# Performance work log

Hardware: AMD Instinct MI355X
Metric: run time of the kernel (lower is better)

## Reference

```python
import jax, jax.numpy as jnp
import numpy as np

LN_EPS = 1e-5
ATTN_THRESH = 0.0005


def _layernorm(x, g, b):
    mu = jnp.mean(x, axis=-1, keepdims=True)
    var = jnp.mean((x - mu) ** 2, axis=-1, keepdims=True)
    return (x - mu) / jnp.sqrt(var + LN_EPS) * g + b


def setup_inputs() -> dict:
    key = jax.random.key(0)
    ks = jax.random.split(key, 10)
    B, P, X, C = 4, 1024, 8192, 1024
    return {
        "feat": jax.random.normal(ks[0], (B, P, C), dtype=jnp.float32),
        "mem_k": jax.random.normal(ks[1], (B, X, C), dtype=jnp.float32),
        "mem_v": jax.random.normal(ks[2], (B, X, C), dtype=jnp.float32),
        "mem_c": jax.random.uniform(ks[3], (B, X, 1), dtype=jnp.float32),
        "mem_attn": jnp.zeros((B, X, 1), dtype=jnp.float32),
        "g_q": jax.random.uniform(ks[4], (C,), dtype=jnp.float32, minval=0.5, maxval=1.5),
        "b_q": jax.random.normal(ks[5], (C,), dtype=jnp.float32) * 0.02,
        "g_k": jax.random.uniform(ks[6], (C,), dtype=jnp.float32, minval=0.5, maxval=1.5),
        "b_k": jax.random.normal(ks[7], (C,), dtype=jnp.float32) * 0.02,
        "g_v": jax.random.uniform(ks[8], (C,), dtype=jnp.float32, minval=0.5, maxval=1.5),
        "b_v": jax.random.normal(ks[9], (C,), dtype=jnp.float32) * 0.02,
    }


def reference(feat, mem_k, mem_v, mem_c, mem_attn, g_q, b_q, g_k, b_k, g_v, b_v):
    # SpatialMemory.memory_read with res=True
    C = feat.shape[-1]
    q = _layernorm(feat, g_q, b_q)                      # [B,P,C]
    k = _layernorm(mem_k, g_k, b_k)                     # [B,X,C]
    affinity = jnp.einsum('bpc,bxc->bpx', q, k)
    affinity = affinity / jnp.sqrt(jnp.asarray(C, jnp.float32))
    # confidence scaling: mem_c viewed as [B,1,X]
    affinity = affinity * jnp.swapaxes(mem_c, 1, 2)
    attn = jax.nn.softmax(affinity, axis=-1)            # [B,P,X]
    # threshold sparsify + renormalize
    attn = jnp.where(attn < ATTN_THRESH, jnp.zeros((), attn.dtype), attn)
    attn = attn / jnp.sum(attn, axis=-1, keepdims=True)
    v = _layernorm(mem_v, g_v, b_v)                     # [B,X,C]
    out = jnp.einsum('bpx,bxc->bpc', attn, v) + feat    # residual
    return out
```

## Files before the change

### kernel.cpp

```cpp
#include <hip/hip_runtime.h>

typedef __attribute__((ext_vector_type(8))) _Float16 half8;
typedef __attribute__((ext_vector_type(4))) _Float16 half4v;
typedef __attribute__((ext_vector_type(4))) float f32x4;

__device__ __forceinline__ void gll16(const void* g, void* l) {
  __builtin_amdgcn_global_load_lds(
      (const __attribute__((address_space(1))) unsigned int*)g,
      (__attribute__((address_space(3))) unsigned int*)l, 16, 0, 0);
}

__global__ __launch_bounds__(256) void ln_cast_f16(
    const float* __restrict__ x, const float* __restrict__ g,
    const float* __restrict__ b, _Float16* __restrict__ y) {
  const int C = 1024;
  size_t row = blockIdx.x;
  int t = threadIdx.x;
  const float4* xr = (const float4*)(x + row * C);
  float4 v = xr[t];
  float s = v.x + v.y + v.z + v.w;
  float s2 = v.x * v.x + v.y * v.y + v.z * v.z + v.w * v.w;
#pragma unroll
  for (int off = 1; off < 64; off <<= 1) {
    s += __shfl_xor(s, off, 64);
    s2 += __shfl_xor(s2, off, 64);
  }
  __shared__ float ps[4], ps2[4];
  int wave = t >> 6, lane = t & 63;
  if (lane == 0) { ps[wave] = s; ps2[wave] = s2; }
  __syncthreads();
  s = ps[0] + ps[1] + ps[2] + ps[3];
  s2 = ps2[0] + ps2[1] + ps2[2] + ps2[3];
  float mu = s * (1.0f / C);
  float var = s2 * (1.0f / C) - mu * mu;
  float rstd = rsqrtf(var + 1e-5f);
  float4 gv = ((const float4*)g)[t];
  float4 bv = ((const float4*)b)[t];
  half4v o;
  o.x = (_Float16)((v.x - mu) * rstd * gv.x + bv.x);
  o.y = (_Float16)((v.y - mu) * rstd * gv.y + bv.y);
  o.z = (_Float16)((v.z - mu) * rstd * gv.z + bv.z);
  o.w = (_Float16)((v.w - mu) * rstd * gv.w + bv.w);
  ((half4v*)(y + row * C))[t] = o;
}

__global__ __launch_bounds__(256) void gemm_bt_f16(
    const _Float16* __restrict__ A,
    const _Float16* __restrict__ Bm,
    float* __restrict__ Cm,
    int M, int N, int K,
    const float* __restrict__ colscale,
    float scale)
{
  int bz = blockIdx.z;
  const _Float16* Ab = A + (size_t)bz * M * K;
  const _Float16* Bb = Bm + (size_t)bz * N * K;
  float* Cb = Cm + (size_t)bz * M * N;

  __shared__ _Float16 lA[128 * 32];
  __shared__ _Float16 lB[128 * 32];

  int tid = threadIdx.x;
  int wave = tid >> 6, lane = tid & 63;
  int wm = wave >> 1, wn = wave & 1;
  int m0 = blockIdx.y * 128, n0 = blockIdx.x * 128;

  f32x4 acc[4][4];
  f32x4 zero = {0.f, 0.f, 0.f, 0.f};
#pragma unroll
  for (int i = 0; i < 4; ++i)
#pragma unroll
    for (int j = 0; j < 4; ++j) acc[i][j] = zero;

  int seg0 = wave * 2, seg1 = wave * 2 + 1;
  int row0 = (seg0 & 1) * 64 + lane, kc0 = seg0 >> 1;
  int row1 = (seg1 & 1) * 64 + lane, kc1 = seg1 >> 1;

  const _Float16* gA0 = Ab + (size_t)(m0 + row0) * K + kc0 * 8;
  const _Float16* gA1 = Ab + (size_t)(m0 + row1) * K + kc1 * 8;
  const _Float16* gB0 = Bb + (size_t)(n0 + row0) * K + kc0 * 8;
  const _Float16* gB1 = Bb + (size_t)(n0 + row1) * K + kc1 * 8;
  _Float16* dA0 = &lA[seg0 * 512 + lane * 8];
  _Float16* dA1 = &lA[seg1 * 512 + lane * 8];
  _Float16* dB0 = &lB[seg0 * 512 + lane * 8];
  _Float16* dB1 = &lB[seg1 * 512 + lane * 8];

  int kg = lane >> 4, lr = lane & 15;

  for (int k0 = 0; k0 < K; k0 += 32) {
    __syncthreads();
    gll16(gA0 + k0, dA0);
    gll16(gA1 + k0, dA1);
    gll16(gB0 + k0, dB0);
    gll16(gB1 + k0, dB1);
    __syncthreads();
    half8 af[4], bfr[4];
#pragma unroll
    for (int t = 0; t < 4; ++t) {
      int m = wm * 64 + t * 16 + lr;
      af[t] = *(const half8*)&lA[kg * 1024 + m * 8];
      int n = wn * 64 + t * 16 + lr;
      bfr[t] = *(const half8*)&lB[kg * 1024 + n * 8];
    }
#pragma unroll
    for (int t = 0; t < 4; ++t)
#pragma unroll
      for (int u = 0; u < 4; ++u)
        acc[t][u] = __builtin_amdgcn_mfma_f32_16x16x32_f16(af[t], bfr[u], acc[t][u], 0, 0, 0);
  }

  int cq = lane >> 4, cn = lane & 15;
  const float* csb = colscale ? colscale + (size_t)bz * N : nullptr;
#pragma unroll
  for (int u = 0; u < 4; ++u) {
    int gn = n0 + wn * 64 + u * 16 + cn;
    float cs = scale * (csb ? csb[gn] : 1.0f);
#pragma unroll
    for (int t = 0; t < 4; ++t) {
      int gm = m0 + wm * 64 + t * 16 + cq * 4;
#pragma unroll
      for (int r = 0; r < 4; ++r) {
        size_t idx = (size_t)(gm + r) * N + gn;
        Cb[idx] = acc[t][u][r] * cs;
      }
    }
  }
}

__global__ __launch_bounds__(256) void softmax_compact(
    const float* __restrict__ S, unsigned* __restrict__ entries,
    int* __restrict__ counts) {
  const int X = 8192;
  size_t row = blockIdx.x;
  const float4* sr = (const float4*)(S + row * X);
  int t = threadIdx.x;
  int wave = t >> 6, lane = t & 63;
  __shared__ float sh[4];
  __shared__ int scnt;
  float4 v[8];
#pragma unroll
  for (int j = 0; j < 8; ++j) v[j] = sr[t + j * 256];

  float m = -1e30f;
#pragma unroll
  for (int j = 0; j < 8; ++j)
    m = fmaxf(m, fmaxf(fmaxf(v[j].x, v[j].y), fmaxf(v[j].z, v[j].w)));
#pragma unroll
  for (int off = 1; off < 64; off <<= 1) m = fmaxf(m, __shfl_xor(m, off, 64));
  if (lane == 0) sh[wave] = m;
  __syncthreads();
  m = fmaxf(fmaxf(sh[0], sh[1]), fmaxf(sh[2], sh[3]));
  __syncthreads();

  float l = 0.f;
#pragma unroll
  for (int j = 0; j < 8; ++j) {
    v[j].x = __expf(v[j].x - m);
    v[j].y = __expf(v[j].y - m);
    v[j].z = __expf(v[j].z - m);
    v[j].w = __expf(v[j].w - m);
    l += v[j].x + v[j].y + v[j].z + v[j].w;
  }
#pragma unroll
  for (int off = 1; off < 64; off <<= 1) l += __shfl_xor(l, off, 64);
  if (lane == 0) sh[wave] = l;
  __syncthreads();
  l = sh[0] + sh[1] + sh[2] + sh[3];
  __syncthreads();

  float thr = 0.0005f * l;
  float ks = 0.f;
#pragma unroll
  for (int j = 0; j < 8; ++j) {
    v[j].x = (v[j].x >= thr) ? v[j].x : 0.f;
    v[j].y = (v[j].y >= thr) ? v[j].y : 0.f;
    v[j].z = (v[j].z >= thr) ? v[j].z : 0.f;
    v[j].w = (v[j].w >= thr) ? v[j].w : 0.f;
    ks += v[j].x + v[j].y + v[j].z + v[j].w;
  }
#pragma unroll
  for (int off = 1; off < 64; off <<= 1) ks += __shfl_xor(ks, off, 64);
  if (lane == 0) sh[wave] = ks;
  __syncthreads();
  if (t == 0) scnt = 0;
  __syncthreads();
  ks = sh[0] + sh[1] + sh[2] + sh[3];

  float inv = 1.0f / ks;
  unsigned* er = entries + row * 2048;
#pragma unroll
  for (int j = 0; j < 8; ++j) {
    int cbase = (t + j * 256) * 4;
    float vals[4] = {v[j].x, v[j].y, v[j].z, v[j].w};
#pragma unroll
    for (int c = 0; c < 4; ++c) {
      if (vals[c] > 0.f) {
        int pos = atomicAdd(&scnt, 1);
        _Float16 h = (_Float16)(vals[c] * inv);
        unsigned short hb;
        __builtin_memcpy(&hb, &h, 2);
        er[pos] = ((unsigned)(cbase + c) << 16) | hb;
      }
    }
  }
  __syncthreads();
  if (t == 0) counts[row] = scnt;
}

__global__ __launch_bounds__(256) void gather_pv(
    const unsigned* __restrict__ entries, const int* __restrict__ counts,
    const _Float16* __restrict__ v16, const float* __restrict__ feat,
    float* __restrict__ out) {
  const int X = 8192, C = 1024;
  int row = blockIdx.x;
  int b = row >> 10;
  const unsigned* er = entries + (size_t)row * 2048;
  int cnt = counts[row];
  int t = threadIdx.x;
  const _Float16* vb = v16 + (size_t)b * X * C;

  float4 acc = {0.f, 0.f, 0.f, 0.f};
  __shared__ unsigned se[256];

  for (int base = 0; base < cnt; base += 256) {
    int n = min(256, cnt - base);
    __syncthreads();
    if (t < n) se[t] = er[base + t];
    __syncthreads();
#pragma unroll 8
    for (int j = 0; j < n; ++j) {
      unsigned e = se[j];
      int x = e >> 16;
      unsigned short hb = (unsigned short)(e & 0xffff);
      _Float16 h;
      __builtin_memcpy(&h, &hb, 2);
      float w = (float)h;
      half4v vv = *(const half4v*)(vb + (size_t)x * C + t * 4);
      acc.x += w * (float)vv.x;
      acc.y += w * (float)vv.y;
      acc.z += w * (float)vv.z;
      acc.w += w * (float)vv.w;
    }
  }
  size_t o = (size_t)row * C + t * 4;
  float4 f = *(const float4*)(feat + o);
  acc.x += f.x; acc.y += f.y; acc.z += f.z; acc.w += f.w;
  *(float4*)(out + o) = acc;
}

extern "C" void kernel_launch(void* const* d_in, const int* in_sizes, int n_in,
                              void* d_out, int out_size, void* d_ws, size_t ws_size,
                              hipStream_t stream) {
  const int B = 4, P = 1024, X = 8192, C = 1024;
  const float* feat  = (const float*)d_in[0];
  const float* mem_k = (const float*)d_in[1];
  const float* mem_v = (const float*)d_in[2];
  const float* mem_c = (const float*)d_in[3];
  const float* g_q = (const float*)d_in[5];
  const float* b_q = (const float*)d_in[6];
  const float* g_k = (const float*)d_in[7];
  const float* b_k = (const float*)d_in[8];
  const float* g_v = (const float*)d_in[9];
  const float* b_v = (const float*)d_in[10];

  char* ws = (char*)d_ws;
  const size_t MB = 1024 * 1024;
  _Float16* q16 = (_Float16*)(ws + 0);
  _Float16* k16 = (_Float16*)(ws + 8 * MB);
  _Float16* v16 = (_Float16*)(ws + 72 * MB);
  float*    S   = (float*)(ws + 136 * MB);
  unsigned* entries = (unsigned*)(ws + 264 * MB);
  int*      counts  = (int*)(ws + 296 * MB);

  ln_cast_f16<<<B * P, 256, 0, stream>>>(feat, g_q, b_q, q16);
  ln_cast_f16<<<B * X, 256, 0, stream>>>(mem_k, g_k, b_k, k16);
  ln_cast_f16<<<B * X, 256, 0, stream>>>(mem_v, g_v, b_v, v16);
  gemm_bt_f16<<<dim3(X / 128, P / 128, B), 256, 0, stream>>>(
      q16, k16, S, P, X, C, mem_c, 0.03125f);
  softmax_compact<<<B * P, 256, 0, stream>>>(S, entries, counts);
  gather_pv<<<B * P, 256, 0, stream>>>(entries, counts, v16, feat, (float*)d_out);
}
```

Baseline: 573.3 us.

## Store scores in fp16, enlarge QK GEMM tile, split gather across waves

The score matrix is now written and read as fp16 instead of fp32, which halves the main intermediate traffic between the GEMM and the softmax kernel. The GEMM tile grows to 256x128 with 512 threads so each K tile of the memory keys is reused across more query rows. The gather kernel loads all entries into shared memory once, splits them across four thread groups using 8-wide half loads, and reduces the partial sums in LDS. The risk is fp16 precision loss in the scores before the softmax and threshold, which could flip entries near the threshold.

After: 538.3 us. 6.1% less time.

```diff
diff --git a/kernel.cpp b/kernel.cpp
--- a/kernel.cpp
+++ b/kernel.cpp
@@ -8,6 +8,12 @@
   __builtin_amdgcn_global_load_lds(
       (const __attribute__((address_space(1))) unsigned int*)g,
       (__attribute__((address_space(3))) unsigned int*)l, 16, 0, 0);
+}
+
+__device__ __forceinline__ float h2f(unsigned short hb) {
+  _Float16 h;
+  __builtin_memcpy(&h, &hb, 2);
+  return (float)h;
 }
 
 __global__ __launch_bounds__(256) void ln_cast_f16(
@@ -44,26 +50,25 @@
   ((half4v*)(y + row * C))[t] = o;
 }
 
-__global__ __launch_bounds__(256) void gemm_bt_f16(
+__global__ __launch_bounds__(512) void gemm_qk_f16(
     const _Float16* __restrict__ A,
     const _Float16* __restrict__ Bm,
-    float* __restrict__ Cm,
-    int M, int N, int K,
-    const float* __restrict__ colscale,
-    float scale)
+    _Float16* __restrict__ Sm,
+    const float* __restrict__ conf)
 {
+  const int M = 1024, N = 8192, K = 1024;
   int bz = blockIdx.z;
   const _Float16* Ab = A + (size_t)bz * M * K;
   const _Float16* Bb = Bm + (size_t)bz * N * K;
-  float* Cb = Cm + (size_t)bz * M * N;
-
-  __shared__ _Float16 lA[128 * 32];
+  _Float16* Sb = Sm + (size_t)bz * M * N;
+
+  __shared__ _Float16 lA[256 * 32];
   __shared__ _Float16 lB[128 * 32];
 
   int tid = threadIdx.x;
   int wave = tid >> 6, lane = tid & 63;
   int wm = wave >> 1, wn = wave & 1;
-  int m0 = blockIdx.y * 128, n0 = blockIdx.x * 128;
+  int m0 = blockIdx.y * 256, n0 = blockIdx.x * 128;
 
   f32x4 acc[4][4];
   f32x4 zero = {0.f, 0.f, 0.f, 0.f};
@@ -72,18 +77,15 @@
 #pragma unroll
     for (int j = 0; j < 4; ++j) acc[i][j] = zero;
 
-  int seg0 = wave * 2, seg1 = wave * 2 + 1;
-  int row0 = (seg0 & 1) * 64 + lane, kc0 = seg0 >> 1;
-  int row1 = (seg1 & 1) * 64 + lane, kc1 = seg1 >> 1;
-
-  const _Float16* gA0 = Ab + (size_t)(m0 + row0) * K + kc0 * 8;
-  const _Float16* gA1 = Ab + (size_t)(m0 + row1) * K + kc1 * 8;
-  const _Float16* gB0 = Bb + (size_t)(n0 + row0) * K + kc0 * 8;
-  const _Float16* gB1 = Bb + (size_t)(n0 + row1) * K + kc1 * 8;
-  _Float16* dA0 = &lA[seg0 * 512 + lane * 8];
-  _Float16* dA1 = &lA[seg1 * 512 + lane * 8];
-  _Float16* dB0 = &lB[seg0 * 512 + lane * 8];
-  _Float16* dB1 = &lB[seg1 * 512 + lane * 8];
+  int rA0 = tid & 255, kgA0 = tid >> 8;
+  int rA1 = rA0, kgA1 = kgA0 + 2;
+  int rB = tid & 127, kgB = tid >> 7;
+  const _Float16* gA0 = Ab + (size_t)(m0 + rA0) * K + kgA0 * 8;
+  const _Float16* gA1 = Ab + (size_t)(m0 + rA1) * K + kgA1 * 8;
+  const _Float16* gB0 = Bb + (size_t)(n0 + rB) * K + kgB * 8;
+  _Float16* dA0 = &lA[kgA0 * 2048 + rA0 * 8];
+  _Float16* dA1 = &lA[kgA1 * 2048 + rA1 * 8];
+  _Float16* dB0 = &lB[kgB * 1024 + rB * 8];
 
   int kg = lane >> 4, lr = lane & 15;
 
@@ -92,13 +94,12 @@
     gll16(gA0 + k0, dA0);
     gll16(gA1 + k0, dA1);
     gll16(gB0 + k0, dB0);
-    gll16(gB1 + k0, dB1);
     __syncthreads();
     half8 af[4], bfr[4];
 #pragma unroll
     for (int t = 0; t < 4; ++t) {
       int m = wm * 64 + t * 16 + lr;
-      af[t] = *(const half8*)&lA[kg * 1024 + m * 8];
+      af[t] = *(const half8*)&lA[kg * 2048 + m * 8];
       int n = wn * 64 + t * 16 + lr;
       bfr[t] = *(const half8*)&lB[kg * 1024 + n * 8];
     }
@@ -110,41 +111,43 @@
   }
 
   int cq = lane >> 4, cn = lane & 15;
-  const float* csb = colscale ? colscale + (size_t)bz * N : nullptr;
+  const float* cb = conf + (size_t)bz * N;
 #pragma unroll
   for (int u = 0; u < 4; ++u) {
     int gn = n0 + wn * 64 + u * 16 + cn;
-    float cs = scale * (csb ? csb[gn] : 1.0f);
+    float cs = 0.03125f * cb[gn];
 #pragma unroll
     for (int t = 0; t < 4; ++t) {
       int gm = m0 + wm * 64 + t * 16 + cq * 4;
 #pragma unroll
-      for (int r = 0; r < 4; ++r) {
-        size_t idx = (size_t)(gm + r) * N + gn;
-        Cb[idx] = acc[t][u][r] * cs;
-      }
+      for (int r = 0; r < 4; ++r)
+        Sb[(size_t)(gm + r) * N + gn] = (_Float16)(acc[t][u][r] * cs);
     }
   }
 }
 
 __global__ __launch_bounds__(256) void softmax_compact(
-    const float* __restrict__ S, unsigned* __restrict__ entries,
+    const _Float16* __restrict__ S, unsigned* __restrict__ entries,
     int* __restrict__ counts) {
   const int X = 8192;
   size_t row = blockIdx.x;
-  const float4* sr = (const float4*)(S + row * X);
+  const half8* sr = (const half8*)(S + row * X);
   int t = threadIdx.x;
   int wave = t >> 6, lane = t & 63;
   __shared__ float sh[4];
   __shared__ int scnt;
-  float4 v[8];
-#pragma unroll
-  for (int j = 0; j < 8; ++j) v[j] = sr[t + j * 256];
+
+  float v[32];
+#pragma unroll
+  for (int j = 0; j < 4; ++j) {
+    half8 h = sr[t + j * 256];
+#pragma unroll
+    for (int c = 0; c < 8; ++c) v[j * 8 + c] = (float)h[c];
+  }
 
   float m = -1e30f;
 #pragma unroll
-  for (int j = 0; j < 8; ++j)
-    m = fmaxf(m, fmaxf(fmaxf(v[j].x, v[j].y), fmaxf(v[j].z, v[j].w)));
+  for (int i = 0; i < 32; ++i) m = fmaxf(m, v[i]);
 #pragma unroll
   for (int off = 1; off < 64; off <<= 1) m = fmaxf(m, __shfl_xor(m, off, 64));
   if (lane == 0) sh[wave] = m;
@@ -154,12 +157,9 @@
 
   float l = 0.f;
 #pragma unroll
-  for (int j = 0; j < 8; ++j) {
-    v[j].x = __expf(v[j].x - m);
-    v[j].y = __expf(v[j].y - m);
-    v[j].z = __expf(v[j].z - m);
-    v[j].w = __expf(v[j].w - m);
-    l += v[j].x + v[j].y + v[j].z + v[j].w;
+  for (int i = 0; i < 32; ++i) {
+    v[i] = __expf(v[i] - m);
+    l += v[i];
   }
 #pragma unroll
   for (int off = 1; off < 64; off <<= 1) l += __shfl_xor(l, off, 64);
@@ -171,12 +171,9 @@
   float thr = 0.0005f * l;
   float ks = 0.f;
 #pragma unroll
-  for (int j = 0; j < 8; ++j) {
-    v[j].x = (v[j].x >= thr) ? v[j].x : 0.f;
-    v[j].y = (v[j].y >= thr) ? v[j].y : 0.f;
-    v[j].z = (v[j].z >= thr) ? v[j].z : 0.f;
-    v[j].w = (v[j].w >= thr) ? v[j].w : 0.f;
-    ks += v[j].x + v[j].y + v[j].z + v[j].w;
+  for (int i = 0; i < 32; ++i) {
+    v[i] = (v[i] >= thr) ? v[i] : 0.f;
+    ks += v[i];
   }
 #pragma unroll
   for (int off = 1; off < 64; off <<= 1) ks += __shfl_xor(ks, off, 64);
@@ -189,17 +186,16 @@
   float inv = 1.0f / ks;
   unsigned* er = entries + row * 2048;
 #pragma unroll
-  for (int j = 0; j < 8; ++j) {
-    int cbase = (t + j * 256) * 4;
-    float vals[4] = {v[j].x, v[j].y, v[j].z, v[j].w};
-#pragma unroll
-    for (int c = 0; c < 4; ++c) {
-      if (vals[c] > 0.f) {
+  for (int j = 0; j < 4; ++j) {
+#pragma unroll
+    for (int c = 0; c < 8; ++c) {
+      float val = v[j * 8 + c];
+      if (val > 0.f) {
         int pos = atomicAdd(&scnt, 1);
-        _Float16 h = (_Float16)(vals[c] * inv);
+        _Float16 h = (_Float16)(val * inv);
         unsigned short hb;
         __builtin_memcpy(&hb, &h, 2);
-        er[pos] = ((unsigned)(cbase + c) << 16) | hb;
+        er[pos] = ((unsigned)((t + j * 256) * 8 + c) << 16) | hb;
       }
     }
   }
@@ -207,45 +203,49 @@
   if (t == 0) counts[row] = scnt;
 }
 
-__global__ __launch_bounds__(256) void gather_pv(
+__global__ __launch_bounds__(512) void gather_pv(
     const unsigned* __restrict__ entries, const int* __restrict__ counts,
     const _Float16* __restrict__ v16, const float* __restrict__ feat,
     float* __restrict__ out) {
   const int X = 8192, C = 1024;
   int row = blockIdx.x;
   int b = row >> 10;
+  int t = threadIdx.x;
+  int s = t >> 7;
+  int c = (t & 127) * 8;
+
+  __shared__ unsigned se[2048];
+  __shared__ float red[4][1024];
+
+  int cnt = counts[row];
   const unsigned* er = entries + (size_t)row * 2048;
-  int cnt = counts[row];
-  int t = threadIdx.x;
+  for (int i = t; i < cnt; i += 512) se[i] = er[i];
+  __syncthreads();
+
   const _Float16* vb = v16 + (size_t)b * X * C;
-
-  float4 acc = {0.f, 0.f, 0.f, 0.f};
-  __shared__ unsigned se[256];
-
-  for (int base = 0; base < cnt; base += 256) {
-    int n = min(256, cnt - base);
-    __syncthreads();
-    if (t < n) se[t] = er[base + t];
-    __syncthreads();
-#pragma unroll 8
-    for (int j = 0; j < n; ++j) {
-      unsigned e = se[j];
-      int x = e >> 16;
-      unsigned short hb = (unsigned short)(e & 0xffff);
-      _Float16 h;
-      __builtin_memcpy(&h, &hb, 2);
-      float w = (float)h;
-      half4v vv = *(const half4v*)(vb + (size_t)x * C + t * 4);
-      acc.x += w * (float)vv.x;
-      acc.y += w * (float)vv.y;
-      acc.z += w * (float)vv.z;
-      acc.w += w * (float)vv.w;
-    }
-  }
-  size_t o = (size_t)row * C + t * 4;
-  float4 f = *(const float4*)(feat + o);
-  acc.x += f.x; acc.y += f.y; acc.z += f.z; acc.w += f.w;
-  *(float4*)(out + o) = acc;
+  float a0 = 0, a1 = 0, a2 = 0, a3 = 0, a4 = 0, a5 = 0, a6 = 0, a7 = 0;
+#pragma unroll 4
+  for (int j = s; j < cnt; j += 4) {
+    unsigned e = se[j];
+    int x = e >> 16;
+    float w = h2f((unsigned short)(e & 0xffff));
+    half8 vv = *(const half8*)(vb + (size_t)x * C + c);
+    a0 += w * (float)vv[0]; a1 += w * (float)vv[1];
+    a2 += w * (float)vv[2]; a3 += w * (float)vv[3];
+    a4 += w * (float)vv[4]; a5 += w * (float)vv[5];
+    a6 += w * (float)vv[6]; a7 += w * (float)vv[7];
+  }
+  float* rp = &red[s][c];
+  rp[0] = a0; rp[1] = a1; rp[2] = a2; rp[3] = a3;
+  rp[4] = a4; rp[5] = a5; rp[6] = a6; rp[7] = a7;
+  __syncthreads();
+
+  int p = t * 2;
+  float2 f = *(const float2*)(feat + (size_t)row * C + p);
+  float2 o;
+  o.x = red[0][p] + red[1][p] + red[2][p] + red[3][p] + f.x;
+  o.y = red[0][p + 1] + red[1][p + 1] + red[2][p + 1] + red[3][p + 1] + f.y;
+  *(float2*)(out + (size_t)row * C + p) = o;
 }
 
 extern "C" void kernel_launch(void* const* d_in, const int* in_sizes, int n_in,
@@ -268,15 +268,14 @@
   _Float16* q16 = (_Float16*)(ws + 0);
   _Float16* k16 = (_Float16*)(ws + 8 * MB);
   _Float16* v16 = (_Float16*)(ws + 72 * MB);
-  float*    S   = (float*)(ws + 136 * MB);
-  unsigned* entries = (unsigned*)(ws + 264 * MB);
-  int*      counts  = (int*)(ws + 296 * MB);
+  _Float16* S   = (_Float16*)(ws + 136 * MB);
+  unsigned* entries = (unsigned*)(ws + 200 * MB);
+  int*      counts  = (int*)(ws + 232 * MB);
 
   ln_cast_f16<<<B * P, 256, 0, stream>>>(feat, g_q, b_q, q16);
   ln_cast_f16<<<B * X, 256, 0, stream>>>(mem_k, g_k, b_k, k16);
   ln_cast_f16<<<B * X, 256, 0, stream>>>(mem_v, g_v, b_v, v16);
-  gemm_bt_f16<<<dim3(X / 128, P / 128, B), 256, 0, stream>>>(
-      q16, k16, S, P, X, C, mem_c, 0.03125f);
+  gemm_qk_f16<<<dim3(X / 128, P / 256, B), 512, 0, stream>>>(q16, k16, S, mem_c);
   softmax_compact<<<B * P, 256, 0, stream>>>(S, entries, counts);
-  gather_pv<<<B * P, 256, 0, stream>>>(entries, counts, v16, feat, (float*)d_out);
-}
+  gather_pv<<<B * P, 512, 0, stream>>>(entries, counts, v16, feat, (float*)d_out);
+}
```
